# Kernel tuning notes

Hardware: AMD Instinct MI355X
Metric: run time of the kernel (lower is better)

## Reference

```python
import jax, jax.numpy as jnp
import numpy as np
import math

EMBED_DIM = 768
NUM_FRAMES = 48
NUM_FREQS = 10
C_IN = 3
FOURIER_DIM = 4 * NUM_FREQS  # include_uv=False
PM_HID = C_IN * 9 * 4        # patch_mlp_ratio=4
OM_HID = EMBED_DIM * 4       # out_mlp_ratio=4
B, N, T, H, W = 4, 8192, 48, 256, 256


def setup_inputs() -> dict:
    key = jax.random.key(0)
    ks = jax.random.split(key, 16)
    uv = jax.random.uniform(ks[0], (B, N, 2), dtype=jnp.float32)
    ts = jax.random.randint(ks[1], (B, N, 3), 0, NUM_FRAMES).astype(jnp.float32)
    query = jnp.concatenate([uv, ts], axis=-1)  # (B,N,5)
    images = jax.random.normal(ks[2], (B, C_IN, T, H, W), dtype=jnp.float32)
    def xavier(k, fan_in, fan_out):
        lim = math.sqrt(6.0 / (fan_in + fan_out))
        return jax.random.uniform(k, (fan_in, fan_out), dtype=jnp.float32, minval=-lim, maxval=lim)
    return {
        "query": query,
        "images": images,
        "uv_w": xavier(ks[3], FOURIER_DIM, EMBED_DIM),
        "uv_b": jnp.zeros((EMBED_DIM,), jnp.float32),
        "t_src_emb": 0.02 * jax.random.normal(ks[4], (NUM_FRAMES, EMBED_DIM), dtype=jnp.float32),
        "t_tgt_emb": 0.02 * jax.random.normal(ks[5], (NUM_FRAMES, EMBED_DIM), dtype=jnp.float32),
        "t_cam_emb": 0.02 * jax.random.normal(ks[6], (NUM_FRAMES, EMBED_DIM), dtype=jnp.float32),
        "pm_w1": xavier(ks[7], C_IN * 9, PM_HID),
        "pm_b1": jnp.zeros((PM_HID,), jnp.float32),
        "pm_w2": xavier(ks[8], PM_HID, EMBED_DIM),
        "pm_b2": jnp.zeros((EMBED_DIM,), jnp.float32),
        "om_w1": xavier(ks[9], EMBED_DIM, OM_HID),
        "om_b1": jnp.zeros((OM_HID,), jnp.float32),
        "om_w2": xavier(ks[10], OM_HID, EMBED_DIM),
        "om_b2": jnp.zeros((EMBED_DIM,), jnp.float32),
    }


def reference(query, images, uv_w, uv_b, t_src_emb, t_tgt_emb, t_cam_emb,
              pm_w1, pm_b1, pm_w2, pm_b2, om_w1, om_b1, om_w2, om_b2):
    # images: (B,C,T,H,W) -> (B,T,C,H,W)
    images = jnp.transpose(images, (0, 2, 1, 3, 4))
    Bq, Nq, _ = query.shape
    _, Tq, C, Hh, Ww = images.shape

    uv = jnp.clip(query[..., 0:2].astype(jnp.float32), 0.0, 1.0)  # (B,N,2)
    t_src = jnp.clip(jnp.round(query[..., 2]).astype(jnp.int32), 0, NUM_FRAMES - 1)
    t_tgt = jnp.clip(jnp.round(query[..., 3]).astype(jnp.int32), 0, NUM_FRAMES - 1)
    t_cam = jnp.clip(jnp.round(query[..., 4]).astype(jnp.int32), 0, NUM_FRAMES - 1)

    # Fourier features of (u,v)
    fb = 2.0 ** jnp.arange(NUM_FREQS, dtype=jnp.float32)  # (F,)
    u = uv[..., 0:1]
    v = uv[..., 1:2]
    up = (2.0 * math.pi) * u * fb  # (B,N,F)
    vp = (2.0 * math.pi) * v * fb
    feat = jnp.concatenate([jnp.sin(up), jnp.cos(up), jnp.sin(vp), jnp.cos(vp)], axis=-1)

    token1 = feat @ uv_w + uv_b              # (B,N,D)
    token2 = t_src_emb[t_src]                # embedding lookups
    token3 = t_tgt_emb[t_tgt]
    token4 = t_cam_emb[t_cam]

    # 3x3 patch gather centered at discrete (u,v) pixel of frame t_src
    x = jnp.round(uv[..., 0] * (Ww - 1)).astype(jnp.int32)  # (B,N)
    y = jnp.round(uv[..., 1] * (Hh - 1)).astype(jnp.int32)
    d = jnp.arange(-1, 2, dtype=jnp.int32)
    x_idx = jnp.clip(x[..., None] + d, 0, Ww - 1)  # (B,N,3)
    y_idx = jnp.clip(y[..., None] + d, 0, Hh - 1)  # (B,N,3)
    b_idx = jnp.arange(Bq)[:, None, None, None, None]
    c_idx = jnp.arange(C)[:, None, None]
    # direct fancy-index gather -> (B,N,C,3,3); avoids materializing (B,N,C,H,W)
    patches = images[b_idx,
                     t_src[:, :, None, None, None],
                     c_idx,
                     y_idx[:, :, None, :, None],
                     x_idx[:, :, None, None, :]]
    patch_flat = patches.reshape(Bq, Nq, C * 9)

    h = jax.nn.gelu(patch_flat @ pm_w1 + pm_b1, approximate=False)
    token5 = h @ pm_w2 + pm_b2

    out = token1 + token2 + token3 + token4 + token5
    out = jax.nn.gelu(out @ om_w1 + om_b1, approximate=False) @ om_w2 + om_b2
    return out
```

## Files before the change

kernel.cpp:

```cpp
#include <hip/hip_runtime.h>

typedef __bf16 bf16x8 __attribute__((ext_vector_type(8)));
typedef float  f32x4  __attribute__((ext_vector_type(4)));

#define GAS(p) ((const __attribute__((address_space(1))) void*)(p))
#define LAS(p) ((__attribute__((address_space(3))) void*)(p))

__device__ __forceinline__ float gelu_exact(float x) {
    return 0.5f * x * (1.f + erff(x * 0.70710678118654752440f));
}

__global__ __launch_bounds__(256) void stage1_kernel(
    const float* __restrict__ query, const float* __restrict__ images,
    const float* __restrict__ pm_w1, const float* __restrict__ pm_b1,
    __bf16* __restrict__ G, int* __restrict__ tbuf)
{
    __shared__ float patch[4][28];
    const int wave = threadIdx.x >> 6, lane = threadIdx.x & 63;
    const int p = blockIdx.x * 4 + wave;
    const float* q = query + (size_t)p * 5;
    float u = fminf(fmaxf(q[0], 0.f), 1.f);
    float v = fminf(fmaxf(q[1], 0.f), 1.f);
    int ts = min(max((int)rintf(q[2]), 0), 47);
    int tt = min(max((int)rintf(q[3]), 0), 47);
    int tc = min(max((int)rintf(q[4]), 0), 47);
    const int b = p >> 13;
    if (lane < 27) {
        int c = lane / 9, rem = lane % 9, dy = rem / 3, dx = rem % 3;
        int x = (int)rintf(u * 255.f), y = (int)rintf(v * 255.f);
        int xx = min(max(x + dx - 1, 0), 255);
        int yy = min(max(y + dy - 1, 0), 255);
        size_t idx = ((size_t)((b * 3 + c) * 48 + ts) << 16) + ((size_t)yy << 8) + (size_t)xx;
        patch[wave][lane] = images[idx];
    }
    if (lane < 40) {
        int i = lane % 10;
        float base = (lane < 20) ? u : v;
        float ph = 6.28318530717958647693f * base * exp2f((float)i);
        float val = ((lane / 10) & 1) ? cosf(ph) : sinf(ph);
        G[(size_t)p * 192 + lane] = (__bf16)val;
    }
    for (int j = 148 + lane; j < 192; j += 64) G[(size_t)p * 192 + j] = (__bf16)0.f;
    if (lane < 3) tbuf[p * 3 + lane] = (lane == 0) ? ts : (lane == 1) ? tt : tc;
    __syncthreads();
    for (int j = lane; j < 108; j += 64) {
        float acc = pm_b1[j];
        #pragma unroll
        for (int i2 = 0; i2 < 27; i2++)
            acc = fmaf(patch[wave][i2], pm_w1[i2 * 108 + j], acc);
        G[(size_t)p * 192 + 40 + j] = (__bf16)gelu_exact(acc);
    }
}

__global__ __launch_bounds__(256) void transpose_to_bf16(
    const float* __restrict__ src, __bf16* __restrict__ dst, int R, int C)
{
    __shared__ float t[32][33];
    const int c0 = blockIdx.x * 32, r0 = blockIdx.y * 32;
    const int tx = threadIdx.x & 31, ty = threadIdx.x >> 5;
    #pragma unroll
    for (int i = 0; i < 32; i += 8)
        t[ty + i][tx] = src[(size_t)(r0 + ty + i) * C + (c0 + tx)];
    __syncthreads();
    #pragma unroll
    for (int i = 0; i < 32; i += 8)
        dst[(size_t)(c0 + ty + i) * R + (r0 + tx)] = (__bf16)t[tx][ty + i];
}

__global__ __launch_bounds__(256) void build_wcat(
    const float* __restrict__ uv_w, const float* __restrict__ pm_w2, __bf16* __restrict__ Wt)
{
    int idx = blockIdx.x * 256 + threadIdx.x;
    int n = idx / 192, k = idx % 192;
    float v = 0.f;
    if (k < 40) v = uv_w[k * 768 + n];
    else if (k < 148) v = pm_w2[(k - 40) * 768 + n];
    Wt[idx] = (__bf16)v;
}

enum { EPI_X = 0, EPI_GELU = 1, EPI_OUT = 2 };

template <int EPI, typename OutT>
__global__ __launch_bounds__(256) void gemm_bt(
    const __bf16* __restrict__ A, const __bf16* __restrict__ Bt, int K,
    const float* __restrict__ bias, const float* __restrict__ bias2,
    const int* __restrict__ tbuf,
    const float* __restrict__ e0, const float* __restrict__ e1, const float* __restrict__ e2,
    OutT* __restrict__ Cmat, int N)
{
    __shared__ __attribute__((aligned(16))) __bf16 As[128 * 64];
    __shared__ __attribute__((aligned(16))) __bf16 Bs[128 * 64];
    const int tid = threadIdx.x;
    const int wave = tid >> 6, lane = tid & 63;
    const int wr = wave >> 1, wc = wave & 1;
    const int quad = lane >> 4, l15 = lane & 15;
    const int sw = l15 & 7;

    const int ntiles = N >> 7;
    const int per_super = ntiles << 3;
    const int id = blockIdx.x;
    const int sup = id / per_super, rem = id - sup * per_super;
    const long m0 = (long)(sup * 8 + (rem & 7)) << 7;
    const long n0 = (long)(rem >> 3) << 7;

    f32x4 acc[4][4];
    #pragma unroll
    for (int i = 0; i < 4; i++)
        #pragma unroll
        for (int j = 0; j < 4; j++)
            #pragma unroll
            for (int r = 0; r < 4; r++)
                acc[i][j][r] = 0.f;

    const __bf16* pa[4]; const __bf16* pb[4];
    __bf16* la[4]; __bf16* lb[4];
    #pragma unroll
    for (int t = 0; t < 4; t++) {
        int c = (t * 4 + wave) * 64 + lane;
        int row = c >> 3, s = c & 7, g = s ^ (row & 7);
        pa[t] = A  + (m0 + row) * (long)K + g * 8;
        pb[t] = Bt + (n0 + row) * (long)K + g * 8;
        la[t] = As + (t * 4 + wave) * 512;
        lb[t] = Bs + (t * 4 + wave) * 512;
    }

    for (int kt = 0; kt < K; kt += 64) {
        #pragma unroll
        for (int t = 0; t < 4; t++) {
            __builtin_amdgcn_global_load_lds(GAS(pa[t] + kt), LAS(la[t]), 16, 0, 0);
            __builtin_amdgcn_global_load_lds(GAS(pb[t] + kt), LAS(lb[t]), 16, 0, 0);
        }
        __syncthreads();
        #pragma unroll
        for (int h = 0; h < 2; h++) {
            const int slot = ((h * 4 + quad) ^ sw) * 8;
            bf16x8 af[4], bfv[4];
            #pragma unroll
            for (int i = 0; i < 4; i++)
                af[i] = *(const bf16x8*)&As[(wr * 64 + i * 16 + l15) * 64 + slot];
            #pragma unroll
            for (int j = 0; j < 4; j++)
                bfv[j] = *(const bf16x8*)&Bs[(wc * 64 + j * 16 + l15) * 64 + slot];
            #pragma unroll
            for (int i = 0; i < 4; i++)
                #pragma unroll
                for (int j = 0; j < 4; j++)
                    acc[i][j] = __builtin_amdgcn_mfma_f32_16x16x32_bf16(af[i], bfv[j], acc[i][j], 0, 0, 0);
        }
        __syncthreads();
    }

    #pragma unroll
    for (int i = 0; i < 4; i++) {
        #pragma unroll
        for (int r = 0; r < 4; r++) {
            long row = m0 + wr * 64 + i * 16 + quad * 4 + r;
            int t0 = 0, t1 = 0, t2 = 0;
            if constexpr (EPI == EPI_X) {
                t0 = tbuf[row * 3 + 0];
                t1 = tbuf[row * 3 + 1];
                t2 = tbuf[row * 3 + 2];
            }
            #pragma unroll
            for (int j = 0; j < 4; j++) {
                long col = n0 + wc * 64 + j * 16 + l15;
                float val = acc[i][j][r];
                if constexpr (EPI == EPI_X) {
                    val += bias[col] + bias2[col];
                    val += e0[t0 * 768 + col] + e1[t1 * 768 + col] + e2[t2 * 768 + col];
                    Cmat[row * (long)N + col] = (OutT)val;
                } else if constexpr (EPI == EPI_GELU) {
                    val += bias[col];
                    Cmat[row * (long)N + col] = (OutT)gelu_exact(val);
                } else {
                    val += bias[col];
                    Cmat[row * (long)N + col] = (OutT)val;
                }
            }
        }
    }
}

static constexpr size_t OFF_G  = 0;
static constexpr size_t OFF_T  = 12582912;
static constexpr size_t OFF_WC = 12976128;
static constexpr size_t OFF_W1 = 13271040;
static constexpr size_t OFF_W2 = 17989632;
static constexpr size_t OFF_X  = 22708224;
static constexpr size_t OFF_H2 = 73039872;

extern "C" void kernel_launch(void* const* d_in, const int* in_sizes, int n_in,
                              void* d_out, int out_size, void* d_ws, size_t ws_size,
                              hipStream_t stream)
{
    const float* query  = (const float*)d_in[0];
    const float* images = (const float*)d_in[1];
    const float* uv_w   = (const float*)d_in[2];
    const float* uv_b   = (const float*)d_in[3];
    const float* e_src  = (const float*)d_in[4];
    const float* e_tgt  = (const float*)d_in[5];
    const float* e_cam  = (const float*)d_in[6];
    const float* pm_w1  = (const float*)d_in[7];
    const float* pm_b1  = (const float*)d_in[8];
    const float* pm_w2  = (const float*)d_in[9];
    const float* pm_b2  = (const float*)d_in[10];
    const float* om_w1  = (const float*)d_in[11];
    const float* om_b1  = (const float*)d_in[12];
    const float* om_w2  = (const float*)d_in[13];
    const float* om_b2  = (const float*)d_in[14];
    float* out = (float*)d_out;
    char* ws = (char*)d_ws;

    __bf16* G    = (__bf16*)(ws + OFF_G);
    int*    tb   = (int*)(ws + OFF_T);
    __bf16* Wcat = (__bf16*)(ws + OFF_WC);
    __bf16* W1t  = (__bf16*)(ws + OFF_W1);
    __bf16* W2t  = (__bf16*)(ws + OFF_W2);
    __bf16* X    = (__bf16*)(ws + OFF_X);
    __bf16* H2   = (__bf16*)(ws + OFF_H2);

    stage1_kernel<<<8192, 256, 0, stream>>>(query, images, pm_w1, pm_b1, G, tb);
    transpose_to_bf16<<<dim3(3072 / 32, 768 / 32), 256, 0, stream>>>(om_w1, W1t, 768, 3072);
    transpose_to_bf16<<<dim3(768 / 32, 3072 / 32), 256, 0, stream>>>(om_w2, W2t, 3072, 768);
    build_wcat<<<576, 256, 0, stream>>>(uv_w, pm_w2, Wcat);

    gemm_bt<EPI_X, __bf16><<<256 * 6, 256, 0, stream>>>(
        G, Wcat, 192, uv_b, pm_b2, tb, e_src, e_tgt, e_cam, X, 768);

    long Mc = 1024;
    for (long cand = 32768; cand >= 1024; cand >>= 1)
        if (OFF_H2 + (size_t)cand * 3072 * 2 <= ws_size) { Mc = cand; break; }

    for (long m = 0; m < 32768; m += Mc) {
        gemm_bt<EPI_GELU, __bf16><<<(Mc / 128) * 24, 256, 0, stream>>>(
            X + m * 768, W1t, 768, om_b1, nullptr, nullptr, nullptr, nullptr, nullptr, H2, 3072);
        gemm_bt<EPI_OUT, float><<<(Mc / 128) * 6, 256, 0, stream>>>(
            H2, W2t, 3072, om_b2, nullptr, nullptr, nullptr, nullptr, nullptr, out + m * 768, 768);
    }
}
```

Baseline: 705.5 us.

## Switch GEMM to 32x32x16 MFMA with 256x128 tiles and fragment-ordered LDS

Replaces the 16x16x32 bf16 MFMA with the 32x32x16 variant and doubles the block M tile to 256 rows, so each wave computes a 128x64 output with larger instructions. The LDS layout changes from an XOR-swizzled row-major tile to a per-lane fragment-ordered layout, so each lane's operand is a contiguous 16-byte read. Launch bounds request 3 blocks per CU and grid sizes are halved to match. The aim is higher MFMA throughput and fewer LDS reads per FLOP, at the cost of more LDS (48KB) and accumulator registers per block, which can limit occupancy.

Result: slower. 1.064 ms (+50.8%).

```diff
diff --git a/kernel.cpp b/kernel.cpp
--- a/kernel.cpp
+++ b/kernel.cpp
@@ -1,7 +1,7 @@
 #include <hip/hip_runtime.h>
 
 typedef __bf16 bf16x8 __attribute__((ext_vector_type(8)));
-typedef float  f32x4  __attribute__((ext_vector_type(4)));
+typedef float  f32x16 __attribute__((ext_vector_type(16)));
 
 #define GAS(p) ((const __attribute__((address_space(1))) void*)(p))
 #define LAS(p) ((__attribute__((address_space(3))) void*)(p))
@@ -81,80 +81,78 @@
 enum { EPI_X = 0, EPI_GELU = 1, EPI_OUT = 2 };
 
 template <int EPI, typename OutT>
-__global__ __launch_bounds__(256) void gemm_bt(
+__global__ __launch_bounds__(256, 3) void gemm_bt(
     const __bf16* __restrict__ A, const __bf16* __restrict__ Bt, int K,
     const float* __restrict__ bias, const float* __restrict__ bias2,
     const int* __restrict__ tbuf,
     const float* __restrict__ e0, const float* __restrict__ e1, const float* __restrict__ e2,
     OutT* __restrict__ Cmat, int N)
 {
-    __shared__ __attribute__((aligned(16))) __bf16 As[128 * 64];
+    __shared__ __attribute__((aligned(16))) __bf16 As[256 * 64];
     __shared__ __attribute__((aligned(16))) __bf16 Bs[128 * 64];
     const int tid = threadIdx.x;
-    const int wave = tid >> 6, lane = tid & 63;
-    const int wr = wave >> 1, wc = wave & 1;
-    const int quad = lane >> 4, l15 = lane & 15;
-    const int sw = l15 & 7;
+    const int w = tid >> 6, lane = tid & 63;
+    const int wr = w >> 1, wc = w & 1;
+    const int l31 = lane & 31, half = lane >> 5;
 
     const int ntiles = N >> 7;
     const int per_super = ntiles << 3;
     const int id = blockIdx.x;
     const int sup = id / per_super, rem = id - sup * per_super;
-    const long m0 = (long)(sup * 8 + (rem & 7)) << 7;
+    const long m0 = (long)(sup * 8 + (rem & 7)) << 8;
     const long n0 = (long)(rem >> 3) << 7;
 
-    f32x4 acc[4][4];
+    f32x16 acc[4][2];
     #pragma unroll
     for (int i = 0; i < 4; i++)
         #pragma unroll
-        for (int j = 0; j < 4; j++)
-            #pragma unroll
-            for (int r = 0; r < 4; r++)
+        for (int j = 0; j < 2; j++)
+            #pragma unroll
+            for (int r = 0; r < 16; r++)
                 acc[i][j][r] = 0.f;
 
-    const __bf16* pa[4]; const __bf16* pb[4];
-    __bf16* la[4]; __bf16* lb[4];
-    #pragma unroll
-    for (int t = 0; t < 4; t++) {
-        int c = (t * 4 + wave) * 64 + lane;
-        int row = c >> 3, s = c & 7, g = s ^ (row & 7);
-        pa[t] = A  + (m0 + row) * (long)K + g * 8;
-        pb[t] = Bt + (n0 + row) * (long)K + g * 8;
-        la[t] = As + (t * 4 + wave) * 512;
-        lb[t] = Bs + (t * 4 + wave) * 512;
-    }
+    const __bf16* a_lane = A  + (m0 + l31) * (long)K + half * 8;
+    const __bf16* b_lane = Bt + (n0 + l31) * (long)K + half * 8;
 
     for (int kt = 0; kt < K; kt += 64) {
         #pragma unroll
-        for (int t = 0; t < 4; t++) {
-            __builtin_amdgcn_global_load_lds(GAS(pa[t] + kt), LAS(la[t]), 16, 0, 0);
-            __builtin_amdgcn_global_load_lds(GAS(pb[t] + kt), LAS(lb[t]), 16, 0, 0);
+        for (int s = 0; s < 8; s++) {
+            const int slot = w * 8 + s;
+            const int mi = slot >> 2, ks = slot & 3;
+            __builtin_amdgcn_global_load_lds(
+                GAS(a_lane + (long)mi * 32 * K + kt + ks * 16),
+                LAS(As + slot * 512), 16, 0, 0);
+        }
+        #pragma unroll
+        for (int ks = 0; ks < 4; ks++) {
+            __builtin_amdgcn_global_load_lds(
+                GAS(b_lane + (long)w * 32 * K + kt + ks * 16),
+                LAS(Bs + (w * 4 + ks) * 512), 16, 0, 0);
         }
         __syncthreads();
         #pragma unroll
-        for (int h = 0; h < 2; h++) {
-            const int slot = ((h * 4 + quad) ^ sw) * 8;
-            bf16x8 af[4], bfv[4];
-            #pragma unroll
-            for (int i = 0; i < 4; i++)
-                af[i] = *(const bf16x8*)&As[(wr * 64 + i * 16 + l15) * 64 + slot];
-            #pragma unroll
-            for (int j = 0; j < 4; j++)
-                bfv[j] = *(const bf16x8*)&Bs[(wc * 64 + j * 16 + l15) * 64 + slot];
-            #pragma unroll
-            for (int i = 0; i < 4; i++)
+        for (int ks = 0; ks < 4; ks++) {
+            bf16x8 af[4];
+            #pragma unroll
+            for (int mi2 = 0; mi2 < 4; mi2++)
+                af[mi2] = *(const bf16x8*)&As[((wr * 4 + mi2) * 4 + ks) * 512 + lane * 8];
+            #pragma unroll
+            for (int nj2 = 0; nj2 < 2; nj2++) {
+                bf16x8 bfr = *(const bf16x8*)&Bs[((wc * 2 + nj2) * 4 + ks) * 512 + lane * 8];
                 #pragma unroll
-                for (int j = 0; j < 4; j++)
-                    acc[i][j] = __builtin_amdgcn_mfma_f32_16x16x32_bf16(af[i], bfv[j], acc[i][j], 0, 0, 0);
+                for (int mi2 = 0; mi2 < 4; mi2++)
+                    acc[mi2][nj2] = __builtin_amdgcn_mfma_f32_32x32x16_bf16(
+                        af[mi2], bfr, acc[mi2][nj2], 0, 0, 0);
+            }
         }
         __syncthreads();
     }
 
     #pragma unroll
-    for (int i = 0; i < 4; i++) {
-        #pragma unroll
-        for (int r = 0; r < 4; r++) {
-            long row = m0 + wr * 64 + i * 16 + quad * 4 + r;
+    for (int mi2 = 0; mi2 < 4; mi2++) {
+        #pragma unroll
+        for (int r = 0; r < 16; r++) {
+            const long row = m0 + (wr * 4 + mi2) * 32 + (r & 3) + ((r >> 2) & 3) * 8 + half * 4;
             int t0 = 0, t1 = 0, t2 = 0;
             if constexpr (EPI == EPI_X) {
                 t0 = tbuf[row * 3 + 0];
@@ -162,9 +160,9 @@
                 t2 = tbuf[row * 3 + 2];
             }
             #pragma unroll
-            for (int j = 0; j < 4; j++) {
-                long col = n0 + wc * 64 + j * 16 + l15;
-                float val = acc[i][j][r];
+            for (int nj2 = 0; nj2 < 2; nj2++) {
+                const long col = n0 + (wc * 2 + nj2) * 32 + l31;
+                float val = acc[mi2][nj2][r];
                 if constexpr (EPI == EPI_X) {
                     val += bias[col] + bias2[col];
                     val += e0[t0 * 768 + col] + e1[t1 * 768 + col] + e2[t2 * 768 + col];
@@ -224,17 +222,17 @@
     transpose_to_bf16<<<dim3(768 / 32, 3072 / 32), 256, 0, stream>>>(om_w2, W2t, 3072, 768);
     build_wcat<<<576, 256, 0, stream>>>(uv_w, pm_w2, Wcat);
 
-    gemm_bt<EPI_X, __bf16><<<256 * 6, 256, 0, stream>>>(
+    gemm_bt<EPI_X, __bf16><<<128 * 6, 256, 0, stream>>>(
         G, Wcat, 192, uv_b, pm_b2, tb, e_src, e_tgt, e_cam, X, 768);
 
-    long Mc = 1024;
-    for (long cand = 32768; cand >= 1024; cand >>= 1)
+    long Mc = 2048;
+    for (long cand = 32768; cand >= 2048; cand >>= 1)
         if (OFF_H2 + (size_t)cand * 3072 * 2 <= ws_size) { Mc = cand; break; }
 
     for (long m = 0; m < 32768; m += Mc) {
-        gemm_bt<EPI_GELU, __bf16><<<(Mc / 128) * 24, 256, 0, stream>>>(
+        gemm_bt<EPI_GELU, __bf16><<<(Mc / 256) * 24, 256, 0, stream>>>(
             X + m * 768, W1t, 768, om_b1, nullptr, nullptr, nullptr, nullptr, nullptr, H2, 3072);
-        gemm_bt<EPI_OUT, float><<<(Mc / 128) * 6, 256, 0, stream>>>(
+        gemm_bt<EPI_OUT, float><<<(Mc / 256) * 6, 256, 0, stream>>>(
             H2, W2t, 3072, om_b2, nullptr, nullptr, nullptr, nullptr, nullptr, out + m * 768, 768);
     }
 }
```

## Replace LDS-staged GEMM tiles with direct register double-buffered global loads

Applied to the files above, without the earlier changes.

Drops the shared-memory staging in the bf16 MFMA GEMM. Each wave now loads its A and B fragments straight from global memory into registers, double-buffered across 32-wide K steps, with no barriers. Launch bounds now request 3 blocks per SM. This removes the LDS round trip and the __syncthreads stalls, but tiles shared between waves are no longer reused. Each block reads A and B twice from global memory/L2, and the loads are 16-byte strided rows that coalesce poorly.

Result: slower. 1.376 ms (+95.0%).

```diff
diff --git a/kernel.cpp b/kernel.cpp
--- a/kernel.cpp
+++ b/kernel.cpp
@@ -2,9 +2,6 @@
 
 typedef __bf16 bf16x8 __attribute__((ext_vector_type(8)));
 typedef float  f32x4  __attribute__((ext_vector_type(4)));
-
-#define GAS(p) ((const __attribute__((address_space(1))) void*)(p))
-#define LAS(p) ((__attribute__((address_space(3))) void*)(p))
 
 __device__ __forceinline__ float gelu_exact(float x) {
     return 0.5f * x * (1.f + erff(x * 0.70710678118654752440f));
@@ -81,20 +78,17 @@
 enum { EPI_X = 0, EPI_GELU = 1, EPI_OUT = 2 };
 
 template <int EPI, typename OutT>
-__global__ __launch_bounds__(256) void gemm_bt(
+__global__ __launch_bounds__(256, 3) void gemm_bt(
     const __bf16* __restrict__ A, const __bf16* __restrict__ Bt, int K,
     const float* __restrict__ bias, const float* __restrict__ bias2,
     const int* __restrict__ tbuf,
     const float* __restrict__ e0, const float* __restrict__ e1, const float* __restrict__ e2,
     OutT* __restrict__ Cmat, int N)
 {
-    __shared__ __attribute__((aligned(16))) __bf16 As[128 * 64];
-    __shared__ __attribute__((aligned(16))) __bf16 Bs[128 * 64];
     const int tid = threadIdx.x;
-    const int wave = tid >> 6, lane = tid & 63;
-    const int wr = wave >> 1, wc = wave & 1;
+    const int w = tid >> 6, lane = tid & 63;
+    const int wr = w >> 1, wc = w & 1;
     const int quad = lane >> 4, l15 = lane & 15;
-    const int sw = l15 & 7;
 
     const int ntiles = N >> 7;
     const int per_super = ntiles << 3;
@@ -112,43 +106,38 @@
             for (int r = 0; r < 4; r++)
                 acc[i][j][r] = 0.f;
 
-    const __bf16* pa[4]; const __bf16* pb[4];
-    __bf16* la[4]; __bf16* lb[4];
-    #pragma unroll
-    for (int t = 0; t < 4; t++) {
-        int c = (t * 4 + wave) * 64 + lane;
-        int row = c >> 3, s = c & 7, g = s ^ (row & 7);
-        pa[t] = A  + (m0 + row) * (long)K + g * 8;
-        pb[t] = Bt + (n0 + row) * (long)K + g * 8;
-        la[t] = As + (t * 4 + wave) * 512;
-        lb[t] = Bs + (t * 4 + wave) * 512;
-    }
-
-    for (int kt = 0; kt < K; kt += 64) {
-        #pragma unroll
-        for (int t = 0; t < 4; t++) {
-            __builtin_amdgcn_global_load_lds(GAS(pa[t] + kt), LAS(la[t]), 16, 0, 0);
-            __builtin_amdgcn_global_load_lds(GAS(pb[t] + kt), LAS(lb[t]), 16, 0, 0);
+    const __bf16* a_base = A  + (m0 + wr * 64 + l15) * (long)K + quad * 8;
+    const __bf16* b_base = Bt + (n0 + wc * 64 + l15) * (long)K + quad * 8;
+
+    bf16x8 af[2][4], bfv[2][4];
+    #pragma unroll
+    for (int i = 0; i < 4; i++) {
+        af[0][i]  = *(const bf16x8*)(a_base + (long)i * 16 * K);
+        bfv[0][i] = *(const bf16x8*)(b_base + (long)i * 16 * K);
+    }
+
+    int buf = 0;
+    for (int kt = 32; kt < K; kt += 32) {
+        const int nxt = buf ^ 1;
+        #pragma unroll
+        for (int i = 0; i < 4; i++) {
+            af[nxt][i]  = *(const bf16x8*)(a_base + (long)i * 16 * K + kt);
+            bfv[nxt][i] = *(const bf16x8*)(b_base + (long)i * 16 * K + kt);
         }
-        __syncthreads();
-        #pragma unroll
-        for (int h = 0; h < 2; h++) {
-            const int slot = ((h * 4 + quad) ^ sw) * 8;
-            bf16x8 af[4], bfv[4];
-            #pragma unroll
-            for (int i = 0; i < 4; i++)
-                af[i] = *(const bf16x8*)&As[(wr * 64 + i * 16 + l15) * 64 + slot];
+        #pragma unroll
+        for (int i = 0; i < 4; i++)
             #pragma unroll
             for (int j = 0; j < 4; j++)
-                bfv[j] = *(const bf16x8*)&Bs[(wc * 64 + j * 16 + l15) * 64 + slot];
-            #pragma unroll
-            for (int i = 0; i < 4; i++)
-                #pragma unroll
-                for (int j = 0; j < 4; j++)
-                    acc[i][j] = __builtin_amdgcn_mfma_f32_16x16x32_bf16(af[i], bfv[j], acc[i][j], 0, 0, 0);
-        }
-        __syncthreads();
-    }
+                acc[i][j] = __builtin_amdgcn_mfma_f32_16x16x32_bf16(
+                    af[buf][i], bfv[buf][j], acc[i][j], 0, 0, 0);
+        buf = nxt;
+    }
+    #pragma unroll
+    for (int i = 0; i < 4; i++)
+        #pragma unroll
+        for (int j = 0; j < 4; j++)
+            acc[i][j] = __builtin_amdgcn_mfma_f32_16x16x32_bf16(
+                af[buf][i], bfv[buf][j], acc[i][j], 0, 0, 0);
 
     #pragma unroll
     for (int i = 0; i < 4; i++) {
```
